# Kernel tuning notes

Measured on AMD Instinct MI355X. Metric: run time of the kernel, lower is better.

Reference implementation:

```python
import jax, jax.numpy as jnp
import numpy as np

N, E, F_IN, H, G, C = 50000, 800000, 128, 4, 32, 4
NEG_SLOPE = 0.2
EPS_GN = 1e-5


def setup_inputs() -> dict:
    key = jax.random.key(0)
    ks = iter(jax.random.split(key, 64))
    def gl(shape, fan):
        return jax.random.normal(next(ks), shape, jnp.float32) / np.float32(np.sqrt(fan))
    inp = {}
    inp['x'] = jax.random.normal(next(ks), (N, F_IN), jnp.float32)
    inp['edge_index'] = jax.random.randint(next(ks), (2, E), 0, N, dtype=jnp.int32)
    inp['batch'] = jnp.sort(jax.random.randint(next(ks), (N,), 0, G, dtype=jnp.int32))
    inp['Wl1'] = gl((F_IN, H * 64), F_IN); inp['bl1'] = jnp.zeros((H * 64,), jnp.float32)
    inp['Wr1'] = gl((F_IN, H * 64), F_IN); inp['br1'] = jnp.zeros((H * 64,), jnp.float32)
    inp['att1'] = gl((H, 64), 64); inp['bias1'] = jnp.zeros((H * 64,), jnp.float32)
    inp['gw1'] = jnp.ones((H * 64,), jnp.float32); inp['gb1'] = jnp.zeros((H * 64,), jnp.float32); inp['ga1'] = jnp.ones((H * 64,), jnp.float32)
    inp['Wl2'] = gl((256, H * 32), 256); inp['bl2'] = jnp.zeros((H * 32,), jnp.float32)
    inp['Wr2'] = gl((256, H * 32), 256); inp['br2'] = jnp.zeros((H * 32,), jnp.float32)
    inp['att2'] = gl((H, 32), 32); inp['bias2'] = jnp.zeros((H * 32,), jnp.float32)
    inp['gw2'] = jnp.ones((H * 32,), jnp.float32); inp['gb2'] = jnp.zeros((H * 32,), jnp.float32); inp['ga2'] = jnp.ones((H * 32,), jnp.float32)
    # GATv2 layer 3: 128 -> 16, 4 heads averaged (concat=False)
    inp['Wl3'] = gl((128, H * 16), 128); inp['bl3'] = jnp.zeros((H * 16,), jnp.float32)
    inp['Wr3'] = gl((128, H * 16), 128); inp['br3'] = jnp.zeros((H * 16,), jnp.float32)
    inp['att3'] = gl((H, 16), 16); inp['bias3'] = jnp.zeros((16,), jnp.float32)
    inp['gw3'] = jnp.ones((16,), jnp.float32); inp['gb3'] = jnp.zeros((16,), jnp.float32); inp['ga3'] = jnp.ones((16,), jnp.float32)
    # final linear 16 -> C
    inp['linW'] = gl((16, C), 16); inp['linB'] = jnp.zeros((C,), jnp.float32)
    return inp


def _gatv2(x, src, dst, Wl, bl, Wr, br, att, bias, D, concat):
    n = x.shape[0]
    xl = (x @ Wl + bl).reshape(n, H, D)   # source-side transform
    xr = (x @ Wr + br).reshape(n, H, D)   # target-side transform
    m = xl[src] + xr[dst]                  # [E', H, D]
    s = jnp.einsum('ehd,hd->eh', jax.nn.leaky_relu(m, NEG_SLOPE), att)
    smax = jax.ops.segment_max(s, dst, num_segments=n)
    e = jnp.exp(s - smax[dst])
    denom = jax.ops.segment_sum(e, dst, num_segments=n)
    alpha = e / (denom[dst] + 1e-16)       # softmax over incoming edges
    out = jax.ops.segment_sum(alpha[:, :, None] * xl[src], dst, num_segments=n)
    out = out.reshape(n, H * D) if concat else out.mean(axis=1)
    return out + bias


def _graphnorm(x, batch, w, b, a):
    cnt = jnp.maximum(jax.ops.segment_sum(jnp.ones((x.shape[0],), x.dtype), batch, num_segments=G), 1.0)
    mean = jax.ops.segment_sum(x, batch, num_segments=G) / cnt[:, None]
    xc = x - a * mean[batch]
    var = jax.ops.segment_sum(xc * xc, batch, num_segments=G) / cnt[:, None]
    return w * xc / jnp.sqrt(var[batch] + EPS_GN) + b


def reference(x, edge_index, batch,
              Wl1, bl1, Wr1, br1, att1, bias1, gw1, gb1, ga1,
              Wl2, bl2, Wr2, br2, att2, bias2, gw2, gb2, ga2,
              Wl3, bl3, Wr3, br3, att3, bias3, gw3, gb3, ga3,
              linW, linB):
    n = x.shape[0]
    ar = jnp.arange(n, dtype=edge_index.dtype)
    src = jnp.concatenate([edge_index[0], ar])  # add self-loops (PyG default)
    dst = jnp.concatenate([edge_index[1], ar])
    h = jax.nn.relu(_graphnorm(_gatv2(x, src, dst, Wl1, bl1, Wr1, br1, att1, bias1, 64, True), batch, gw1, gb1, ga1))
    h = jax.nn.relu(_graphnorm(_gatv2(h, src, dst, Wl2, bl2, Wr2, br2, att2, bias2, 32, True), batch, gw2, gb2, ga2))
    h = jax.nn.relu(_graphnorm(_gatv2(h, src, dst, Wl3, bl3, Wr3, br3, att3, bias3, 16, False), batch, gw3, gb3, ga3))
    cnt = jnp.maximum(jax.ops.segment_sum(jnp.ones((n,), h.dtype), batch, num_segments=G), 1.0)
    features = jax.ops.segment_sum(h, batch, num_segments=G) / cnt[:, None]  # global mean pool [G,16]
    logits = features @ linW + linB
    return (logits, features)
```

## Files before the change

kernel.cpp:

```cpp
#include <hip/hip_runtime.h>
#include <cstdint>


#define NEG_SLOPE 0.2f

typedef __attribute__((ext_vector_type(8))) short short8;
typedef __attribute__((ext_vector_type(4))) float f32x4;
typedef _Float16 h2 __attribute__((ext_vector_type(2)));
union U16 { uint4 u; short8 s; };

__device__ inline unsigned short f2bf_rne(float x) {
  unsigned u = __float_as_uint(x);
  return (unsigned short)((u + 0x7fff + ((u >> 16) & 1)) >> 16);
}
__device__ inline unsigned short f2h_bits(float x) {
  _Float16 h = (_Float16)x;
  return __builtin_bit_cast(unsigned short, h);
}
__device__ inline float h2f(unsigned short h) {
  return (float)__builtin_bit_cast(_Float16, h);
}
__device__ inline h2 u2h2(unsigned u) { return __builtin_bit_cast(h2, u); }

__device__ inline float fdot2h(h2 a, h2 b, float c) {
#if __has_builtin(__builtin_amdgcn_fdot2)
  return __builtin_amdgcn_fdot2(a, b, c, false);
#else
  return c + (float)a.x * (float)b.x + (float)a.y * (float)b.y;
#endif
}

__device__ inline int wave_incl_scan(int v, int lane) {
#pragma unroll
  for (int ofs = 1; ofs < 64; ofs <<= 1) {
    int t = __shfl_up(v, ofs, 64);
    if (lane >= ofs) v += t;
  }
  return v;
}

__global__ void deg_hist(const int* __restrict__ ei, int* __restrict__ deg, int E, int N) {
  int i = blockIdx.x * blockDim.x + threadIdx.x;
  int ET = E + N;
  if (i >= ET) return;
  int d = (i < E) ? ei[E + i] : (i - E);
  atomicAdd(&deg[d], 1);
}

__global__ void chunk_sums(const int* __restrict__ deg, int* __restrict__ bsum, int n) {
  int tid = threadIdx.x, lane = tid & 63, wid = tid >> 6;
  int i = blockIdx.x * 1024 + tid;
  int v = (i < n) ? deg[i] : 0;
#pragma unroll
  for (int m = 32; m; m >>= 1) v += __shfl_xor(v, m, 64);
  __shared__ int ws[16];
  if (lane == 0) ws[wid] = v;
  __syncthreads();
  if (tid == 0) {
    int s = 0;
    for (int k = 0; k < 16; ++k) s += ws[k];
    bsum[blockIdx.x] = s;
  }
}

__global__ void scan_small(int* __restrict__ bsum, int* __restrict__ off, int nb, int n) {
  int lane = threadIdx.x;
  int v = (lane < nb) ? bsum[lane] : 0;
  int orig = v;
  int incl = wave_incl_scan(v, lane);
  if (lane < nb) bsum[lane] = incl - orig;
  if (lane == nb - 1) off[n] = incl;
}

__global__ void scan_apply(const int* __restrict__ deg, const int* __restrict__ boff,
                           int* __restrict__ off, int n) {
  int tid = threadIdx.x, lane = tid & 63, wid = tid >> 6;
  int i = blockIdx.x * 1024 + tid;
  int v = (i < n) ? deg[i] : 0;
  int incl = wave_incl_scan(v, lane);
  __shared__ int ws[16];
  if (lane == 63) ws[wid] = incl;
  __syncthreads();
  if (wid == 0) {
    int t = (lane < 16) ? ws[lane] : 0;
    t = wave_incl_scan(t, lane);
    if (lane < 16) ws[lane] = t;
  }
  __syncthreads();
  int wpre = (wid > 0) ? ws[wid - 1] : 0;
  if (i < n) off[i] = boff[blockIdx.x] + wpre + incl - v;
}

__global__ void scatter_edges(const int* __restrict__ ei, const int* __restrict__ off,
                              int* __restrict__ cur, int* __restrict__ csr_src,
                              int E, int N) {
  int i = blockIdx.x * blockDim.x + threadIdx.x;
  int ET = E + N;
  if (i >= ET) return;
  int s, d;
  if (i < E) { s = ei[i]; d = ei[E + i]; } else { s = d = i - E; }
  int pos = off[d] + atomicAdd(&cur[d], 1);
  csr_src[pos] = s;
}

__global__ void batch_hist(const int* __restrict__ batch, int* __restrict__ cnt, int n) {
  __shared__ int h[32];
  if (threadIdx.x < 32) h[threadIdx.x] = 0;
  __syncthreads();
  int i = blockIdx.x * blockDim.x + threadIdx.x;
  if (i < n) atomicAdd(&h[batch[i]], 1);
  __syncthreads();
  if (threadIdx.x < 32 && h[threadIdx.x] > 0) atomicAdd(&cnt[threadIdx.x], h[threadIdx.x]);
}

__global__ void wprep(const float* __restrict__ W, unsigned short* __restrict__ pk,
                      int K, int M) {
  int t = blockIdx.x * blockDim.x + threadIdx.x;
  int nk = K >> 5;
  int total = (M >> 4) * nk * 512;
  if (t >= total) return;
  int j = t & 7;
  int l = (t >> 3) & 63;
  int rest = t >> 9;
  int kc = rest % nk;
  int ct = rest / nk;
  int k = (kc << 5) + ((l >> 4) << 3) + j;
  int col = (ct << 4) + (l & 15);
  float w = W[(size_t)k * M + col];
  unsigned u = __float_as_uint(w);
  unsigned short hi = (unsigned short)(u >> 16);
  float hif = __uint_as_float(u & 0xffff0000u);
  unsigned short lo = f2bf_rne(w - hif);
  unsigned short* dst = pk + ((size_t)(ct * nk + kc) * 64 + l) * 16;
  dst[j] = hi;
  dst[j + 8] = lo;
}

__global__ __launch_bounds__(256) void gemm_mfma_f32a(
    const float* __restrict__ A, const uint4* __restrict__ Wpk,
    const float* __restrict__ bias, unsigned short* __restrict__ C,
    int N, int K, int M) {
  int wv = threadIdx.x >> 6, lane = threadIdx.x & 63;
  int r0 = blockIdx.y * 64 + wv * 16;
  int c0g = blockIdx.x << 2;
  int row = r0 + (lane & 15);
  int kq = (lane >> 4) << 3;
  int nk = K >> 5;
  bool rok = row < N;
  const float* arow = A + (size_t)row * K;
  f32x4 acc[4];
#pragma unroll
  for (int i = 0; i < 4; ++i) acc[i] = (f32x4){0.f, 0.f, 0.f, 0.f};
  for (int kc = 0; kc < nk; ++kc) {
    float av[8];
    if (rok) {
      float4 t0 = *(const float4*)(arow + (kc << 5) + kq);
      float4 t1 = *(const float4*)(arow + (kc << 5) + kq + 4);
      av[0] = t0.x; av[1] = t0.y; av[2] = t0.z; av[3] = t0.w;
      av[4] = t1.x; av[5] = t1.y; av[6] = t1.z; av[7] = t1.w;
    } else {
#pragma unroll
      for (int j = 0; j < 8; ++j) av[j] = 0.f;
    }
    short8 ahi, alo;
#pragma unroll
    for (int j = 0; j < 8; ++j) {
      unsigned u = __float_as_uint(av[j]);
      ahi[j] = (short)(u >> 16);
      float hif = __uint_as_float(u & 0xffff0000u);
      alo[j] = (short)f2bf_rne(av[j] - hif);
    }
#pragma unroll
    for (int ct = 0; ct < 4; ++ct) {
      const uint4* p = Wpk + (((size_t)(c0g + ct) * nk + kc) * 64 + lane) * 2;
      U16 bh, bl;
      bh.u = p[0];
      bl.u = p[1];
      acc[ct] = __builtin_amdgcn_mfma_f32_16x16x32_bf16(alo, bh.s, acc[ct], 0, 0, 0);
      acc[ct] = __builtin_amdgcn_mfma_f32_16x16x32_bf16(ahi, bl.s, acc[ct], 0, 0, 0);
      acc[ct] = __builtin_amdgcn_mfma_f32_16x16x32_bf16(ahi, bh.s, acc[ct], 0, 0, 0);
    }
  }
  int orow0 = r0 + ((lane >> 4) << 2);
  int ocol = (c0g << 4) + (lane & 15);
#pragma unroll
  for (int ct = 0; ct < 4; ++ct) {
    int col = ocol + (ct << 4);
    float bv = bias[col];
#pragma unroll
    for (int r = 0; r < 4; ++r) {
      int gr = orow0 + r;
      if (gr < N) C[(size_t)gr * M + col] = f2h_bits(acc[ct][r] + bv);
    }
  }
}

__global__ __launch_bounds__(256) void gemm_mfma_bf16a(
    const unsigned short* __restrict__ A, const uint4* __restrict__ Wpk,
    const float* __restrict__ bias, unsigned short* __restrict__ C,
    int N, int K, int M) {
  int wv = threadIdx.x >> 6, lane = threadIdx.x & 63;
  int r0 = blockIdx.y * 64 + wv * 16;
  int c0g = blockIdx.x << 2;
  int row = r0 + (lane & 15);
  int kq = (lane >> 4) << 3;
  int nk = K >> 5;
  bool rok = row < N;
  const unsigned short* arow = A + (size_t)row * K;
  f32x4 acc[4];
#pragma unroll
  for (int i = 0; i < 4; ++i) acc[i] = (f32x4){0.f, 0.f, 0.f, 0.f};
  for (int kc = 0; kc < nk; ++kc) {
    short8 a;
    if (rok) {
      a = *(const short8*)(arow + (kc << 5) + kq);
    } else {
#pragma unroll
      for (int j = 0; j < 8; ++j) a[j] = 0;
    }
#pragma unroll
    for (int ct = 0; ct < 4; ++ct) {
      const uint4* p = Wpk + (((size_t)(c0g + ct) * nk + kc) * 64 + lane) * 2;
      U16 bh, bl;
      bh.u = p[0];
      bl.u = p[1];
      acc[ct] = __builtin_amdgcn_mfma_f32_16x16x32_bf16(a, bl.s, acc[ct], 0, 0, 0);
      acc[ct] = __builtin_amdgcn_mfma_f32_16x16x32_bf16(a, bh.s, acc[ct], 0, 0, 0);
    }
  }
  int orow0 = r0 + ((lane >> 4) << 2);
  int ocol = (c0g << 4) + (lane & 15);
#pragma unroll
  for (int ct = 0; ct < 4; ++ct) {
    int col = ocol + (ct << 4);
    float bv = bias[col];
#pragma unroll
    for (int r = 0; r < 4; ++r) {
      int gr = orow0 + r;
      if (gr < N) C[(size_t)gr * M + col] = f2h_bits(acc[ct][r] + bv);
    }
  }
}

template <int VEC> struct EO;

template <> struct EO<4> {
  using R = uint2;
  h2 xr0, xr1, at0, at1, sl;
  __device__ void init(const unsigned short* xrp, const float* ap) {
    uint2 rr = *(const uint2*)xrp;
    xr0 = u2h2(rr.x); xr1 = u2h2(rr.y);
    float4 a = *(const float4*)ap;
    at0 = (h2){(_Float16)a.x, (_Float16)a.y};
    at1 = (h2){(_Float16)a.z, (_Float16)a.w};
    sl = (h2){(_Float16)NEG_SLOPE, (_Float16)NEG_SLOPE};
  }
  static __device__ R ld(const unsigned short* base, size_t off) {
    return *(const uint2*)(base + off);
  }
  __device__ float score(R r) const {
    h2 t0 = u2h2(r.x) + xr0;
    h2 t1 = u2h2(r.y) + xr1;
    t0 = __builtin_elementwise_max(t0, t0 * sl);
    t1 = __builtin_elementwise_max(t1, t1 * sl);
    return fdot2h(t0, at0, fdot2h(t1, at1, 0.f));
  }
  static __device__ void accum(R r, float p, float* o) {
    h2 x0 = u2h2(r.x), x1 = u2h2(r.y);
    o[0] = fmaf(p, (float)x0.x, o[0]);
    o[1] = fmaf(p, (float)x0.y, o[1]);
    o[2] = fmaf(p, (float)x1.x, o[2]);
    o[3] = fmaf(p, (float)x1.y, o[3]);
  }
};

template <> struct EO<2> {
  using R = unsigned;
  h2 xr0, at0, sl;
  __device__ void init(const unsigned short* xrp, const float* ap) {
    xr0 = u2h2(*(const unsigned*)xrp);
    float2 a = *(const float2*)ap;
    at0 = (h2){(_Float16)a.x, (_Float16)a.y};
    sl = (h2){(_Float16)NEG_SLOPE, (_Float16)NEG_SLOPE};
  }
  static __device__ R ld(const unsigned short* base, size_t off) {
    return *(const unsigned*)(base + off);
  }
  __device__ float score(R r) const {
    h2 t0 = u2h2(r) + xr0;
    t0 = __builtin_elementwise_max(t0, t0 * sl);
    return fdot2h(t0, at0, 0.f);
  }
  static __device__ void accum(R r, float p, float* o) {
    h2 x0 = u2h2(r);
    o[0] = fmaf(p, (float)x0.x, o[0]);
    o[1] = fmaf(p, (float)x0.y, o[1]);
  }
};

template <> struct EO<1> {
  using R = unsigned short;
  float xrf, atf;
  __device__ void init(const unsigned short* xrp, const float* ap) {
    xrf = h2f(*xrp);
    atf = *ap;
  }
  static __device__ R ld(const unsigned short* base, size_t off) {
    return base[off];
  }
  __device__ float score(R r) const {
    float t = h2f(r) + xrf;
    float lk = fmaxf(t, NEG_SLOPE * t);
    return lk * atf;
  }
  static __device__ void accum(R r, float p, float* o) {
    o[0] = fmaf(p, h2f(r), o[0]);
  }
};

template <int VEC, bool MEANH, bool OUT16>
__global__ __launch_bounds__(256) void gat_fused(
    const unsigned short* __restrict__ xl, const unsigned short* __restrict__ xr,
    const float* __restrict__ att, const int* __restrict__ csr_src,
    const int* __restrict__ offp, const float* __restrict__ bias,
    void* __restrict__ outv, int n) {
  constexpr int HD = VEC * 64;
  int wave = (int)((blockIdx.x * (size_t)blockDim.x + threadIdx.x) >> 6);
  int lane = threadIdx.x & 63;
  if (wave >= n) return;
  const int f0 = lane * VEC;

  EO<VEC> eo;
  eo.init(xr + (size_t)wave * HD + f0, att + f0);

  float lrun = 0.f;
  float o[VEC];
#pragma unroll
  for (int v = 0; v < VEC; ++v) o[v] = 0.f;

  int beg = __builtin_amdgcn_readfirstlane(offp[wave]);
  int end = __builtin_amdgcn_readfirstlane(offp[wave + 1]);
  int j = beg;
  int endf = beg + ((end - beg) & ~3);

  for (; j < endf; j += 4) {
    int s0 = csr_src[j], s1 = csr_src[j + 1], s2 = csr_src[j + 2], s3 = csr_src[j + 3];
    typename EO<VEC>::R r0 = eo.ld(xl, (size_t)s0 * HD + f0);
    typename EO<VEC>::R r1 = eo.ld(xl, (size_t)s1 * HD + f0);
    typename EO<VEC>::R r2 = eo.ld(xl, (size_t)s2 * HD + f0);
    typename EO<VEC>::R r3 = eo.ld(xl, (size_t)s3 * HD + f0);
    float sc0 = eo.score(r0), sc1 = eo.score(r1), sc2 = eo.score(r2), sc3 = eo.score(r3);
#pragma unroll
    for (int msk = 1; msk <= 8; msk <<= 1) {
      sc0 += __shfl_xor(sc0, msk, 64);
      sc1 += __shfl_xor(sc1, msk, 64);
      sc2 += __shfl_xor(sc2, msk, 64);
      sc3 += __shfl_xor(sc3, msk, 64);
    }
    float p0 = __expf(sc0), p1 = __expf(sc1);
    float p2 = __expf(sc2), p3 = __expf(sc3);
    lrun += (p0 + p1) + (p2 + p3);
    EO<VEC>::accum(r0, p0, o);
    EO<VEC>::accum(r1, p1, o);
    EO<VEC>::accum(r2, p2, o);
    EO<VEC>::accum(r3, p3, o);
  }
  for (; j < end; ++j) {
    int s0 = csr_src[j];
    typename EO<VEC>::R r0 = eo.ld(xl, (size_t)s0 * HD + f0);
    float sc0 = eo.score(r0);
#pragma unroll
    for (int msk = 1; msk <= 8; msk <<= 1) sc0 += __shfl_xor(sc0, msk, 64);
    float p0 = __expf(sc0);
    lrun += p0;
    EO<VEC>::accum(r0, p0, o);
  }

  float invl = 1.f / (lrun + 1e-16f);
  if (!MEANH) {
    if (OUT16) {
      unsigned short* out = (unsigned short*)outv;
#pragma unroll
      for (int v = 0; v < VEC; ++v)
        out[(size_t)wave * HD + f0 + v] = f2h_bits(o[v] * invl + bias[f0 + v]);
    } else {
      float* out = (float*)outv;
#pragma unroll
      for (int v = 0; v < VEC; ++v)
        out[(size_t)wave * HD + f0 + v] = o[v] * invl + bias[f0 + v];
    }
  } else {
    float val = o[0] * invl;
    val += __shfl_xor(val, 16, 64);
    val += __shfl_xor(val, 32, 64);
    val *= 0.25f;
    if (lane < 16) ((float*)outv)[(size_t)wave * 16 + lane] = val + bias[lane];
  }
}

template <int F>
__global__ void gn_stats_h(const unsigned short* __restrict__ x, const int* __restrict__ batch,
                           float* __restrict__ gsum, float* __restrict__ gsqs, int n) {
  constexpr int ROWS = 256 / F;
  int f = threadIdx.x % F;
  int r = threadIdx.x / F;
  int n0 = blockIdx.x * 128;
  float s = 0.f, q = 0.f;
  int curg = -1;
  for (int i = r; i < 128; i += ROWS) {
    int nn = n0 + i;
    if (nn >= n) break;
    int g = batch[nn];
    float v = h2f(x[(size_t)nn * F + f]);
    if (g != curg) {
      if (curg >= 0) { atomicAdd(&gsum[curg * F + f], s); atomicAdd(&gsqs[curg * F + f], q); }
      curg = g; s = 0.f; q = 0.f;
    }
    s += v; q += v * v;
  }
  if (curg >= 0) { atomicAdd(&gsum[curg * F + f], s); atomicAdd(&gsqs[curg * F + f], q); }
}

template <int F>
__global__ void gn_stats(const float* __restrict__ x, const int* __restrict__ batch,
                         float* __restrict__ gsum, float* __restrict__ gsqs, int n) {
  constexpr int ROWS = 256 / F;
  int f = threadIdx.x % F;
  int r = threadIdx.x / F;
  int n0 = blockIdx.x * 128;
  float s = 0.f, q = 0.f;
  int curg = -1;
  for (int i = r; i < 128; i += ROWS) {
    int nn = n0 + i;
    if (nn >= n) break;
    int g = batch[nn];
    float v = x[(size_t)nn * F + f];
    if (g != curg) {
      if (curg >= 0) { atomicAdd(&gsum[curg * F + f], s); atomicAdd(&gsqs[curg * F + f], q); }
      curg = g; s = 0.f; q = 0.f;
    }
    s += v; q += v * v;
  }
  if (curg >= 0) { atomicAdd(&gsum[curg * F + f], s); atomicAdd(&gsqs[curg * F + f], q); }
}

__global__ void gn_final(const float* __restrict__ gsum, const float* __restrict__ gsqs,
                         const int* __restrict__ cnt, const float* __restrict__ ga,
                         float* __restrict__ gmean, float* __restrict__ grstd, int F) {
  int idx = blockIdx.x * blockDim.x + threadIdx.x;
  if (idx >= 32 * F) return;
  int g = idx / F, f = idx % F;
  float c = fmaxf((float)cnt[g], 1.f);
  float mu = gsum[idx] / c;
  float msq = gsqs[idx] / c;
  float a = ga[f];
  float var = msq - (2.f * a - a * a) * mu * mu;
  var = fmaxf(var, 0.f);
  gmean[idx] = mu;
  grstd[idx] = rsqrtf(var + 1e-5f);
}

template <int F>
__global__ void gn_norm_h_bf16(const unsigned short* __restrict__ x, const int* __restrict__ batch,
                               const float* __restrict__ gmean, const float* __restrict__ grstd,
                               const float* __restrict__ gw, const float* __restrict__ gb,
                               const float* __restrict__ ga, unsigned short* __restrict__ xo,
                               int n) {
  int idx = blockIdx.x * blockDim.x + threadIdx.x;
  if (idx >= n * F) return;
  int nn = idx / F;
  int f = idx % F;
  int g = batch[nn];
  float v = h2f(x[idx]);
  float y = gw[f] * (v - ga[f] * gmean[g * F + f]) * grstd[g * F + f] + gb[f];
  xo[idx] = f2bf_rne(fmaxf(y, 0.f));
}

template <int F>
__global__ void gn_norm(float* __restrict__ x, const int* __restrict__ batch,
                        const float* __restrict__ gmean, const float* __restrict__ grstd,
                        const float* __restrict__ gw, const float* __restrict__ gb,
                        const float* __restrict__ ga, int n) {
  int idx = blockIdx.x * blockDim.x + threadIdx.x;
  if (idx >= n * F) return;
  int nn = idx / F;
  int f = idx % F;
  int g = batch[nn];
  float v = x[idx];
  float y = gw[f] * (v - ga[f] * gmean[g * F + f]) * grstd[g * F + f] + gb[f];
  x[idx] = fmaxf(y, 0.f);
}

__global__ void pool_sum(const float* __restrict__ x, const int* __restrict__ batch,
                         float* __restrict__ pooled, int n) {
  int f = threadIdx.x & 15;
  int r = threadIdx.x >> 4;
  int n0 = blockIdx.x * 128;
  float s = 0.f;
  int curg = -1;
  for (int i = r; i < 128; i += 16) {
    int nn = n0 + i;
    if (nn >= n) break;
    int g = batch[nn];
    float v = x[(size_t)nn * 16 + f];
    if (g != curg) {
      if (curg >= 0) atomicAdd(&pooled[curg * 16 + f], s);
      curg = g; s = 0.f;
    }
    s += v;
  }
  if (curg >= 0) atomicAdd(&pooled[curg * 16 + f], s);
}

__global__ void finalize(const float* __restrict__ pooled, const int* __restrict__ cnt,
                         const float* __restrict__ linW, const float* __restrict__ linB,
                         float* __restrict__ out) {
  __shared__ float feat[32 * 16];
  int tid = threadIdx.x;
  {
    int g = tid >> 4;
    float c = fmaxf((float)cnt[g], 1.f);
    float v = pooled[tid] / c;
    feat[tid] = v;
    out[128 + tid] = v;
  }
  __syncthreads();
  if (tid < 128) {
    int g = tid >> 2, c = tid & 3;
    float s = linB[c];
#pragma unroll
    for (int k = 0; k < 16; ++k) s += feat[g * 16 + k] * linW[k * 4 + c];
    out[g * 4 + c] = s;
  }
}

extern "C" void kernel_launch(void* const* d_in, const int* in_sizes, int n_in,
                              void* d_out, int out_size, void* d_ws, size_t ws_size,
                              hipStream_t stream) {
  const float* x     = (const float*)d_in[0];
  const int*   ei    = (const int*)d_in[1];
  const int*   batch = (const int*)d_in[2];
  const float* Wl1 = (const float*)d_in[3];
  const float* bl1 = (const float*)d_in[4];
  const float* Wr1 = (const float*)d_in[5];
  const float* br1 = (const float*)d_in[6];
  const float* att1 = (const float*)d_in[7];
  const float* bias1 = (const float*)d_in[8];
  const float* gw1 = (const float*)d_in[9];
  const float* gb1 = (const float*)d_in[10];
  const float* ga1 = (const float*)d_in[11];
  const float* Wl2 = (const float*)d_in[12];
  const float* bl2 = (const float*)d_in[13];
  const float* Wr2 = (const float*)d_in[14];
  const float* br2 = (const float*)d_in[15];
  const float* att2 = (const float*)d_in[16];
  const float* bias2 = (const float*)d_in[17];
  const float* gw2 = (const float*)d_in[18];
  const float* gb2 = (const float*)d_in[19];
  const float* ga2 = (const float*)d_in[20];
  const float* Wl3 = (const float*)d_in[21];
  const float* bl3 = (const float*)d_in[22];
  const float* Wr3 = (const float*)d_in[23];
  const float* br3 = (const float*)d_in[24];
  const float* att3 = (const float*)d_in[25];
  const float* bias3 = (const float*)d_in[26];
  const float* gw3 = (const float*)d_in[27];
  const float* gb3 = (const float*)d_in[28];
  const float* ga3 = (const float*)d_in[29];
  const float* linW = (const float*)d_in[30];
  const float* linB = (const float*)d_in[31];
  float* out = (float*)d_out;

  const int N  = in_sizes[2];
  const int E  = in_sizes[1] / 2;
  const int ET = E + N;

  char* w = (char*)d_ws;
  float* P = (float*)w;             w += (size_t)N * 256 * 4;
  unsigned short* Ph = (unsigned short*)P;
  unsigned short* Pb = (unsigned short*)w; w += (size_t)N * 256 * 2;
  unsigned short* Qb = (unsigned short*)w; w += (size_t)N * 256 * 2;
  unsigned short* Rb = (unsigned short*)w; w += (size_t)N * 256 * 2;
  int* csr_src = (int*)w;           w += (size_t)ET * 4;
  int* deg  = (int*)w;              w += (size_t)N * 4;
  int* offp = (int*)w;              w += (size_t)(N + 1) * 4;
  int* cur  = (int*)w;              w += (size_t)N * 4;
  int* bsum = (int*)w;              w += 64 * 4;
  int* cnt  = (int*)w;              w += 32 * 4;
  float* gsum  = (float*)w;         w += 32 * 256 * 4;
  float* gsqs  = (float*)w;         w += 32 * 256 * 4;
  float* gmean = (float*)w;         w += 32 * 256 * 4;
  float* grstd = (float*)w;         w += 32 * 256 * 4;
  float* pooled = (float*)w;        w += 512 * 4;
  uintptr_t wal = ((uintptr_t)w + 15) & ~(uintptr_t)15;
  uint4* wpk1l = (uint4*)wal;
  uint4* wpk1r = wpk1l + 8192;
  uint4* wpk2l = wpk1r + 8192;
  uint4* wpk2r = wpk2l + 8192;
  uint4* wpk3l = wpk2r + 8192;
  uint4* wpk3r = wpk3l + 2048;

  (void)hipMemsetAsync(deg, 0, sizeof(int) * N, stream);
  (void)hipMemsetAsync(cur, 0, sizeof(int) * N, stream);
  (void)hipMemsetAsync(cnt, 0, sizeof(int) * 32, stream);
  (void)hipMemsetAsync(pooled, 0, sizeof(float) * 512, stream);

  wprep<<<128, 256, 0, stream>>>(Wl1, (unsigned short*)wpk1l, 128, 256);
  wprep<<<128, 256, 0, stream>>>(Wr1, (unsigned short*)wpk1r, 128, 256);
  wprep<<<128, 256, 0, stream>>>(Wl2, (unsigned short*)wpk2l, 256, 128);
  wprep<<<128, 256, 0, stream>>>(Wr2, (unsigned short*)wpk2r, 256, 128);
  wprep<<<32, 256, 0, stream>>>(Wl3, (unsigned short*)wpk3l, 128, 64);
  wprep<<<32, 256, 0, stream>>>(Wr3, (unsigned short*)wpk3r, 128, 64);

  int nb = (N + 1023) / 1024;
  deg_hist<<<(ET + 255) / 256, 256, 0, stream>>>(ei, deg, E, N);
  chunk_sums<<<nb, 1024, 0, stream>>>(deg, bsum, N);
  scan_small<<<1, 64, 0, stream>>>(bsum, offp, nb, N);
  scan_apply<<<nb, 1024, 0, stream>>>(deg, bsum, offp, N);
  scatter_edges<<<(ET + 255) / 256, 256, 0, stream>>>(ei, offp, cur, csr_src, E, N);
  batch_hist<<<(N + 255) / 256, 256, 0, stream>>>(batch, cnt, N);

  int gry = (N + 63) / 64;
  {
    gemm_mfma_f32a<<<dim3(4, gry), 256, 0, stream>>>(x, wpk1l, bl1, Qb, N, 128, 256);
    gemm_mfma_f32a<<<dim3(4, gry), 256, 0, stream>>>(x, wpk1r, br1, Rb, N, 128, 256);
    gat_fused<4, false, true><<<(N + 3) / 4, 256, 0, stream>>>(Qb, Rb, att1, csr_src, offp, bias1, Ph, N);
    (void)hipMemsetAsync(gsum, 0, sizeof(float) * 2 * 32 * 256, stream);
    gn_stats_h<256><<<(N + 127) / 128, 256, 0, stream>>>(Ph, batch, gsum, gsqs, N);
    gn_final<<<(32 * 256 + 255) / 256, 256, 0, stream>>>(gsum, gsqs, cnt, ga1, gmean, grstd, 256);
    gn_norm_h_bf16<256><<<(int)(((size_t)N * 256 + 255) / 256), 256, 0, stream>>>(Ph, batch, gmean, grstd, gw1, gb1, ga1, Pb, N);
  }
  {
    gemm_mfma_bf16a<<<dim3(2, gry), 256, 0, stream>>>(Pb, wpk2l, bl2, Qb, N, 256, 128);
    gemm_mfma_bf16a<<<dim3(2, gry), 256, 0, stream>>>(Pb, wpk2r, br2, Rb, N, 256, 128);
    gat_fused<2, false, true><<<(N + 3) / 4, 256, 0, stream>>>(Qb, Rb, att2, csr_src, offp, bias2, Ph, N);
    (void)hipMemsetAsync(gsum, 0, sizeof(float) * 2 * 32 * 256, stream);
    gn_stats_h<128><<<(N + 127) / 128, 256, 0, stream>>>(Ph, batch, gsum, gsqs, N);
    gn_final<<<(32 * 128 + 255) / 256, 256, 0, stream>>>(gsum, gsqs, cnt, ga2, gmean, grstd, 128);
    gn_norm_h_bf16<128><<<(int)(((size_t)N * 128 + 255) / 256), 256, 0, stream>>>(Ph, batch, gmean, grstd, gw2, gb2, ga2, Pb, N);
  }
  {
    gemm_mfma_bf16a<<<dim3(1, gry), 256, 0, stream>>>(Pb, wpk3l, bl3, Qb, N, 128, 64);
    gemm_mfma_bf16a<<<dim3(1, gry), 256, 0, stream>>>(Pb, wpk3r, br3, Rb, N, 128, 64);
    gat_fused<1, true, false><<<(N + 3) / 4, 256, 0, stream>>>(Qb, Rb, att3, csr_src, offp, bias3, P, N);
    (void)hipMemsetAsync(gsum, 0, sizeof(float) * 2 * 32 * 256, stream);
    gn_stats<16><<<(N + 127) / 128, 256, 0, stream>>>(P, batch, gsum, gsqs, N);
    gn_final<<<(32 * 16 + 255) / 256, 256, 0, stream>>>(gsum, gsqs, cnt, ga3, gmean, grstd, 16);
    gn_norm<16><<<(int)(((size_t)N * 16 + 255) / 256), 256, 0, stream>>>(P, batch, gmean, grstd, gw3, gb3, ga3, N);
  }
  pool_sum<<<(N + 127) / 128, 256, 0, stream>>>(P, batch, pooled, N);
  finalize<<<1, 512, 0, stream>>>(pooled, cnt, linW, linB, out);
}
```

Measured before the change: 736.4 us.

## Fuse preprocessing kernels, dual-output GEMMs, and inline GraphNorm finalization

Merges the degree and batch histograms, the six weight-prep launches, and the scan kernels, and replaces the separate memsets with one contiguous memset. Each layer's left and right GEMMs now run as one kernel sharing the A loads. GraphNorm stat zeroing moves into gat_fused and gn_final is folded into the normalize kernels. The edge loop is unrolled to 8-edge chunks. The goal is fewer launches and less redundant A traffic, at the cost of more registers in the dual GEMM and recomputing mean and rstd per element.

Result: faster. 663.1 us (-10.0%).

```diff
diff --git a/kernel.cpp b/kernel.cpp
--- a/kernel.cpp
+++ b/kernel.cpp
@@ -39,12 +39,20 @@
   return v;
 }
 
-__global__ void deg_hist(const int* __restrict__ ei, int* __restrict__ deg, int E, int N) {
+__global__ void deg_batch_hist(const int* __restrict__ ei, const int* __restrict__ batch,
+                               int* __restrict__ deg, int* __restrict__ cnt, int E, int N) {
+  __shared__ int h[32];
+  if (threadIdx.x < 32) h[threadIdx.x] = 0;
+  __syncthreads();
   int i = blockIdx.x * blockDim.x + threadIdx.x;
   int ET = E + N;
-  if (i >= ET) return;
-  int d = (i < E) ? ei[E + i] : (i - E);
-  atomicAdd(&deg[d], 1);
+  if (i < ET) {
+    int d = (i < E) ? ei[E + i] : (i - E);
+    atomicAdd(&deg[d], 1);
+  }
+  if (i < N) atomicAdd(&h[batch[i]], 1);
+  __syncthreads();
+  if (threadIdx.x < 32 && h[threadIdx.x] > 0) atomicAdd(&cnt[threadIdx.x], h[threadIdx.x]);
 }
 
 __global__ void chunk_sums(const int* __restrict__ deg, int* __restrict__ bsum, int n) {
@@ -63,22 +71,22 @@
   }
 }
 
-__global__ void scan_small(int* __restrict__ bsum, int* __restrict__ off, int nb, int n) {
-  int lane = threadIdx.x;
-  int v = (lane < nb) ? bsum[lane] : 0;
-  int orig = v;
-  int incl = wave_incl_scan(v, lane);
-  if (lane < nb) bsum[lane] = incl - orig;
-  if (lane == nb - 1) off[n] = incl;
-}
-
-__global__ void scan_apply(const int* __restrict__ deg, const int* __restrict__ boff,
-                           int* __restrict__ off, int n) {
+__global__ void scan_apply(const int* __restrict__ deg, const int* __restrict__ bsum,
+                           int* __restrict__ off, int nb, int n) {
+  __shared__ int ws[16];
+  __shared__ int sb[64];
   int tid = threadIdx.x, lane = tid & 63, wid = tid >> 6;
+  if (wid == 0) {
+    int v = (lane < nb) ? bsum[lane] : 0;
+    int incl = wave_incl_scan(v, lane);
+    sb[lane] = incl;
+  }
+  __syncthreads();
+  int boff = (blockIdx.x > 0) ? sb[blockIdx.x - 1] : 0;
+  if (blockIdx.x == 0 && tid == 0) off[n] = sb[nb - 1];
   int i = blockIdx.x * 1024 + tid;
   int v = (i < n) ? deg[i] : 0;
   int incl = wave_incl_scan(v, lane);
-  __shared__ int ws[16];
   if (lane == 63) ws[wid] = incl;
   __syncthreads();
   if (wid == 0) {
@@ -88,7 +96,7 @@
   }
   __syncthreads();
   int wpre = (wid > 0) ? ws[wid - 1] : 0;
-  if (i < n) off[i] = boff[blockIdx.x] + wpre + incl - v;
+  if (i < n) off[i] = boff + wpre + incl - v;
 }
 
 __global__ void scatter_edges(const int* __restrict__ ei, const int* __restrict__ off,
@@ -103,19 +111,8 @@
   csr_src[pos] = s;
 }
 
-__global__ void batch_hist(const int* __restrict__ batch, int* __restrict__ cnt, int n) {
-  __shared__ int h[32];
-  if (threadIdx.x < 32) h[threadIdx.x] = 0;
-  __syncthreads();
-  int i = blockIdx.x * blockDim.x + threadIdx.x;
-  if (i < n) atomicAdd(&h[batch[i]], 1);
-  __syncthreads();
-  if (threadIdx.x < 32 && h[threadIdx.x] > 0) atomicAdd(&cnt[threadIdx.x], h[threadIdx.x]);
-}
-
-__global__ void wprep(const float* __restrict__ W, unsigned short* __restrict__ pk,
-                      int K, int M) {
-  int t = blockIdx.x * blockDim.x + threadIdx.x;
+__device__ inline void wprep_body(const float* __restrict__ W, unsigned short* __restrict__ pk,
+                                  int K, int M, int t) {
   int nk = K >> 5;
   int total = (M >> 4) * nk * 512;
   if (t >= total) return;
@@ -136,9 +133,26 @@
   dst[j + 8] = lo;
 }
 
-__global__ __launch_bounds__(256) void gemm_mfma_f32a(
-    const float* __restrict__ A, const uint4* __restrict__ Wpk,
-    const float* __restrict__ bias, unsigned short* __restrict__ C,
+__global__ void wprep_all(const float* W0, const float* W1, const float* W2,
+                          const float* W3, const float* W4, const float* W5,
+                          unsigned short* p0, unsigned short* p1, unsigned short* p2,
+                          unsigned short* p3, unsigned short* p4, unsigned short* p5) {
+  int t = blockIdx.x * 256 + threadIdx.x;
+  switch (blockIdx.y) {
+    case 0: wprep_body(W0, p0, 128, 256, t); break;
+    case 1: wprep_body(W1, p1, 128, 256, t); break;
+    case 2: wprep_body(W2, p2, 256, 128, t); break;
+    case 3: wprep_body(W3, p3, 256, 128, t); break;
+    case 4: wprep_body(W4, p4, 128, 64, t); break;
+    default: wprep_body(W5, p5, 128, 64, t); break;
+  }
+}
+
+__global__ __launch_bounds__(256) void gemm_f32a_dual(
+    const float* __restrict__ A,
+    const uint4* __restrict__ WpkL, const uint4* __restrict__ WpkR,
+    const float* __restrict__ biasL, const float* __restrict__ biasR,
+    unsigned short* __restrict__ CL, unsigned short* __restrict__ CR,
     int N, int K, int M) {
   int wv = threadIdx.x >> 6, lane = threadIdx.x & 63;
   int r0 = blockIdx.y * 64 + wv * 16;
@@ -148,9 +162,9 @@
   int nk = K >> 5;
   bool rok = row < N;
   const float* arow = A + (size_t)row * K;
-  f32x4 acc[4];
-#pragma unroll
-  for (int i = 0; i < 4; ++i) acc[i] = (f32x4){0.f, 0.f, 0.f, 0.f};
+  f32x4 accL[4], accR[4];
+#pragma unroll
+  for (int i = 0; i < 4; ++i) { accL[i] = (f32x4){0,0,0,0}; accR[i] = (f32x4){0,0,0,0}; }
   for (int kc = 0; kc < nk; ++kc) {
     float av[8];
     if (rok) {
@@ -172,13 +186,16 @@
     }
 #pragma unroll
     for (int ct = 0; ct < 4; ++ct) {
-      const uint4* p = Wpk + (((size_t)(c0g + ct) * nk + kc) * 64 + lane) * 2;
+      size_t fo = (((size_t)(c0g + ct) * nk + kc) * 64 + lane) * 2;
       U16 bh, bl;
-      bh.u = p[0];
-      bl.u = p[1];
-      acc[ct] = __builtin_amdgcn_mfma_f32_16x16x32_bf16(alo, bh.s, acc[ct], 0, 0, 0);
-      acc[ct] = __builtin_amdgcn_mfma_f32_16x16x32_bf16(ahi, bl.s, acc[ct], 0, 0, 0);
-      acc[ct] = __builtin_amdgcn_mfma_f32_16x16x32_bf16(ahi, bh.s, acc[ct], 0, 0, 0);
+      bh.u = WpkL[fo]; bl.u = WpkL[fo + 1];
+      accL[ct] = __builtin_amdgcn_mfma_f32_16x16x32_bf16(alo, bh.s, accL[ct], 0, 0, 0);
+      accL[ct] = __builtin_amdgcn_mfma_f32_16x16x32_bf16(ahi, bl.s, accL[ct], 0, 0, 0);
+      accL[ct] = __builtin_amdgcn_mfma_f32_16x16x32_bf16(ahi, bh.s, accL[ct], 0, 0, 0);
+      bh.u = WpkR[fo]; bl.u = WpkR[fo + 1];
+      accR[ct] = __builtin_amdgcn_mfma_f32_16x16x32_bf16(alo, bh.s, accR[ct], 0, 0, 0);
+      accR[ct] = __builtin_amdgcn_mfma_f32_16x16x32_bf16(ahi, bl.s, accR[ct], 0, 0, 0);
+      accR[ct] = __builtin_amdgcn_mfma_f32_16x16x32_bf16(ahi, bh.s, accR[ct], 0, 0, 0);
     }
   }
   int orow0 = r0 + ((lane >> 4) << 2);
@@ -186,18 +203,23 @@
 #pragma unroll
   for (int ct = 0; ct < 4; ++ct) {
     int col = ocol + (ct << 4);
-    float bv = bias[col];
+    float bvL = biasL[col], bvR = biasR[col];
 #pragma unroll
     for (int r = 0; r < 4; ++r) {
       int gr = orow0 + r;
-      if (gr < N) C[(size_t)gr * M + col] = f2h_bits(acc[ct][r] + bv);
-    }
-  }
-}
-
-__global__ __launch_bounds__(256) void gemm_mfma_bf16a(
-    const unsigned short* __restrict__ A, const uint4* __restrict__ Wpk,
-    const float* __restrict__ bias, unsigned short* __restrict__ C,
+      if (gr < N) {
+        CL[(size_t)gr * M + col] = f2h_bits(accL[ct][r] + bvL);
+        CR[(size_t)gr * M + col] = f2h_bits(accR[ct][r] + bvR);
+      }
+    }
+  }
+}
+
+__global__ __launch_bounds__(256) void gemm_bf16a_dual(
+    const unsigned short* __restrict__ A,
+    const uint4* __restrict__ WpkL, const uint4* __restrict__ WpkR,
+    const float* __restrict__ biasL, const float* __restrict__ biasR,
+    unsigned short* __restrict__ CL, unsigned short* __restrict__ CR,
     int N, int K, int M) {
   int wv = threadIdx.x >> 6, lane = threadIdx.x & 63;
   int r0 = blockIdx.y * 64 + wv * 16;
@@ -207,9 +229,9 @@
   int nk = K >> 5;
   bool rok = row < N;
   const unsigned short* arow = A + (size_t)row * K;
-  f32x4 acc[4];
-#pragma unroll
-  for (int i = 0; i < 4; ++i) acc[i] = (f32x4){0.f, 0.f, 0.f, 0.f};
+  f32x4 accL[4], accR[4];
+#pragma unroll
+  for (int i = 0; i < 4; ++i) { accL[i] = (f32x4){0,0,0,0}; accR[i] = (f32x4){0,0,0,0}; }
   for (int kc = 0; kc < nk; ++kc) {
     short8 a;
     if (rok) {
@@ -220,12 +242,14 @@
     }
 #pragma unroll
     for (int ct = 0; ct < 4; ++ct) {
-      const uint4* p = Wpk + (((size_t)(c0g + ct) * nk + kc) * 64 + lane) * 2;
+      size_t fo = (((size_t)(c0g + ct) * nk + kc) * 64 + lane) * 2;
       U16 bh, bl;
-      bh.u = p[0];
-      bl.u = p[1];
-      acc[ct] = __builtin_amdgcn_mfma_f32_16x16x32_bf16(a, bl.s, acc[ct], 0, 0, 0);
-      acc[ct] = __builtin_amdgcn_mfma_f32_16x16x32_bf16(a, bh.s, acc[ct], 0, 0, 0);
+      bh.u = WpkL[fo]; bl.u = WpkL[fo + 1];
+      accL[ct] = __builtin_amdgcn_mfma_f32_16x16x32_bf16(a, bl.s, accL[ct], 0, 0, 0);
+      accL[ct] = __builtin_amdgcn_mfma_f32_16x16x32_bf16(a, bh.s, accL[ct], 0, 0, 0);
+      bh.u = WpkR[fo]; bl.u = WpkR[fo + 1];
+      accR[ct] = __builtin_amdgcn_mfma_f32_16x16x32_bf16(a, bl.s, accR[ct], 0, 0, 0);
+      accR[ct] = __builtin_amdgcn_mfma_f32_16x16x32_bf16(a, bh.s, accR[ct], 0, 0, 0);
     }
   }
   int orow0 = r0 + ((lane >> 4) << 2);
@@ -233,11 +257,14 @@
 #pragma unroll
   for (int ct = 0; ct < 4; ++ct) {
     int col = ocol + (ct << 4);
-    float bv = bias[col];
+    float bvL = biasL[col], bvR = biasR[col];
 #pragma unroll
     for (int r = 0; r < 4; ++r) {
       int gr = orow0 + r;
-      if (gr < N) C[(size_t)gr * M + col] = f2h_bits(acc[ct][r] + bv);
+      if (gr < N) {
+        CL[(size_t)gr * M + col] = f2h_bits(accL[ct][r] + bvL);
+        CR[(size_t)gr * M + col] = f2h_bits(accR[ct][r] + bvR);
+      }
     }
   }
 }
@@ -318,13 +345,43 @@
   }
 };
 
+template <int VEC, int C>
+__device__ inline void gat_chunk(const unsigned short* __restrict__ xl,
+                                 const int* __restrict__ csr_src, int j, int f0,
+                                 const EO<VEC>& eo, float& lrun, float* o) {
+  constexpr int HD = VEC * 64;
+  typename EO<VEC>::R r[C];
+#pragma unroll
+  for (int c = 0; c < C; ++c)
+    r[c] = EO<VEC>::ld(xl, (size_t)csr_src[j + c] * HD + f0);
+  float sc[C];
+#pragma unroll
+  for (int c = 0; c < C; ++c) sc[c] = eo.score(r[c]);
+#pragma unroll
+  for (int msk = 1; msk <= 8; msk <<= 1)
+#pragma unroll
+    for (int c = 0; c < C; ++c) sc[c] += __shfl_xor(sc[c], msk, 64);
+  float p[C];
+#pragma unroll
+  for (int c = 0; c < C; ++c) p[c] = __expf(sc[c]);
+#pragma unroll
+  for (int c = 0; c < C; ++c) lrun += p[c];
+#pragma unroll
+  for (int c = 0; c < C; ++c) EO<VEC>::accum(r[c], p[c], o);
+}
+
 template <int VEC, bool MEANH, bool OUT16>
 __global__ __launch_bounds__(256) void gat_fused(
     const unsigned short* __restrict__ xl, const unsigned short* __restrict__ xr,
     const float* __restrict__ att, const int* __restrict__ csr_src,
     const int* __restrict__ offp, const float* __restrict__ bias,
-    void* __restrict__ outv, int n) {
+    void* __restrict__ outv, float* __restrict__ gsz, float* __restrict__ gqz,
+    int n) {
   constexpr int HD = VEC * 64;
+  {
+    int zt = blockIdx.x * 256 + threadIdx.x;
+    if (zt < 32 * 256) { gsz[zt] = 0.f; gqz[zt] = 0.f; }
+  }
   int wave = (int)((blockIdx.x * (size_t)blockDim.x + threadIdx.x) >> 6);
   int lane = threadIdx.x & 63;
   if (wave >= n) return;
@@ -341,40 +398,9 @@
   int beg = __builtin_amdgcn_readfirstlane(offp[wave]);
   int end = __builtin_amdgcn_readfirstlane(offp[wave + 1]);
   int j = beg;
-  int endf = beg + ((end - beg) & ~3);
-
-  for (; j < endf; j += 4) {
-    int s0 = csr_src[j], s1 = csr_src[j + 1], s2 = csr_src[j + 2], s3 = csr_src[j + 3];
-    typename EO<VEC>::R r0 = eo.ld(xl, (size_t)s0 * HD + f0);
-    typename EO<VEC>::R r1 = eo.ld(xl, (size_t)s1 * HD + f0);
-    typename EO<VEC>::R r2 = eo.ld(xl, (size_t)s2 * HD + f0);
-    typename EO<VEC>::R r3 = eo.ld(xl, (size_t)s3 * HD + f0);
-    float sc0 = eo.score(r0), sc1 = eo.score(r1), sc2 = eo.score(r2), sc3 = eo.score(r3);
-#pragma unroll
-    for (int msk = 1; msk <= 8; msk <<= 1) {
-      sc0 += __shfl_xor(sc0, msk, 64);
-      sc1 += __shfl_xor(sc1, msk, 64);
-      sc2 += __shfl_xor(sc2, msk, 64);
-      sc3 += __shfl_xor(sc3, msk, 64);
-    }
-    float p0 = __expf(sc0), p1 = __expf(sc1);
-    float p2 = __expf(sc2), p3 = __expf(sc3);
-    lrun += (p0 + p1) + (p2 + p3);
-    EO<VEC>::accum(r0, p0, o);
-    EO<VEC>::accum(r1, p1, o);
-    EO<VEC>::accum(r2, p2, o);
-    EO<VEC>::accum(r3, p3, o);
-  }
-  for (; j < end; ++j) {
-    int s0 = csr_src[j];
-    typename EO<VEC>::R r0 = eo.ld(xl, (size_t)s0 * HD + f0);
-    float sc0 = eo.score(r0);
-#pragma unroll
-    for (int msk = 1; msk <= 8; msk <<= 1) sc0 += __shfl_xor(sc0, msk, 64);
-    float p0 = __expf(sc0);
-    lrun += p0;
-    EO<VEC>::accum(r0, p0, o);
-  }
+  for (; j + 8 <= end; j += 8) gat_chunk<VEC, 8>(xl, csr_src, j, f0, eo, lrun, o);
+  if (j + 4 <= end) { gat_chunk<VEC, 4>(xl, csr_src, j, f0, eo, lrun, o); j += 4; }
+  for (; j < end; ++j) gat_chunk<VEC, 1>(xl, csr_src, j, f0, eo, lrun, o);
 
   float invl = 1.f / (lrun + 1e-16f);
   if (!MEANH) {
@@ -444,25 +470,10 @@
   if (curg >= 0) { atomicAdd(&gsum[curg * F + f], s); atomicAdd(&gsqs[curg * F + f], q); }
 }
 
-__global__ void gn_final(const float* __restrict__ gsum, const float* __restrict__ gsqs,
-                         const int* __restrict__ cnt, const float* __restrict__ ga,
-                         float* __restrict__ gmean, float* __restrict__ grstd, int F) {
-  int idx = blockIdx.x * blockDim.x + threadIdx.x;
-  if (idx >= 32 * F) return;
-  int g = idx / F, f = idx % F;
-  float c = fmaxf((float)cnt[g], 1.f);
-  float mu = gsum[idx] / c;
-  float msq = gsqs[idx] / c;
-  float a = ga[f];
-  float var = msq - (2.f * a - a * a) * mu * mu;
-  var = fmaxf(var, 0.f);
-  gmean[idx] = mu;
-  grstd[idx] = rsqrtf(var + 1e-5f);
-}
-
 template <int F>
 __global__ void gn_norm_h_bf16(const unsigned short* __restrict__ x, const int* __restrict__ batch,
-                               const float* __restrict__ gmean, const float* __restrict__ grstd,
+                               const float* __restrict__ gsum, const float* __restrict__ gsqs,
+                               const int* __restrict__ cnt,
                                const float* __restrict__ gw, const float* __restrict__ gb,
                                const float* __restrict__ ga, unsigned short* __restrict__ xo,
                                int n) {
@@ -471,14 +482,20 @@
   int nn = idx / F;
   int f = idx % F;
   int g = batch[nn];
+  float c = fmaxf((float)cnt[g], 1.f);
+  float a = ga[f];
+  float mu = gsum[g * F + f] / c;
+  float var = fmaxf(gsqs[g * F + f] / c - (2.f * a - a * a) * mu * mu, 0.f);
+  float rstd = rsqrtf(var + 1e-5f);
   float v = h2f(x[idx]);
-  float y = gw[f] * (v - ga[f] * gmean[g * F + f]) * grstd[g * F + f] + gb[f];
+  float y = gw[f] * (v - a * mu) * rstd + gb[f];
   xo[idx] = f2bf_rne(fmaxf(y, 0.f));
 }
 
 template <int F>
 __global__ void gn_norm(float* __restrict__ x, const int* __restrict__ batch,
-                        const float* __restrict__ gmean, const float* __restrict__ grstd,
+                        const float* __restrict__ gsum, const float* __restrict__ gsqs,
+                        const int* __restrict__ cnt,
                         const float* __restrict__ gw, const float* __restrict__ gb,
                         const float* __restrict__ ga, int n) {
   int idx = blockIdx.x * blockDim.x + threadIdx.x;
@@ -486,8 +503,13 @@
   int nn = idx / F;
   int f = idx % F;
   int g = batch[nn];
+  float c = fmaxf((float)cnt[g], 1.f);
+  float a = ga[f];
+  float mu = gsum[g * F + f] / c;
+  float var = fmaxf(gsqs[g * F + f] / c - (2.f * a - a * a) * mu * mu, 0.f);
+  float rstd = rsqrtf(var + 1e-5f);
   float v = x[idx];
-  float y = gw[f] * (v - ga[f] * gmean[g * F + f]) * grstd[g * F + f] + gb[f];
+  float y = gw[f] * (v - a * mu) * rstd + gb[f];
   x[idx] = fmaxf(y, 0.f);
 }
 
@@ -582,16 +604,16 @@
   unsigned short* Qb = (unsigned short*)w; w += (size_t)N * 256 * 2;
   unsigned short* Rb = (unsigned short*)w; w += (size_t)N * 256 * 2;
   int* csr_src = (int*)w;           w += (size_t)ET * 4;
+  int* offp = (int*)w;              w += (size_t)(N + 1) * 4;
+  int* bsum = (int*)w;              w += 64 * 4;
+  char* z0 = w;
   int* deg  = (int*)w;              w += (size_t)N * 4;
-  int* offp = (int*)w;              w += (size_t)(N + 1) * 4;
   int* cur  = (int*)w;              w += (size_t)N * 4;
-  int* bsum = (int*)w;              w += 64 * 4;
   int* cnt  = (int*)w;              w += 32 * 4;
+  float* pooled = (float*)w;        w += 512 * 4;
   float* gsum  = (float*)w;         w += 32 * 256 * 4;
   float* gsqs  = (float*)w;         w += 32 * 256 * 4;
-  float* gmean = (float*)w;         w += 32 * 256 * 4;
-  float* grstd = (float*)w;         w += 32 * 256 * 4;
-  float* pooled = (float*)w;        w += 512 * 4;
+  size_t zbytes = (size_t)(w - z0);
   uintptr_t wal = ((uintptr_t)w + 15) & ~(uintptr_t)15;
   uint4* wpk1l = (uint4*)wal;
   uint4* wpk1r = wpk1l + 8192;
@@ -600,53 +622,38 @@
   uint4* wpk3l = wpk2r + 8192;
   uint4* wpk3r = wpk3l + 2048;
 
-  (void)hipMemsetAsync(deg, 0, sizeof(int) * N, stream);
-  (void)hipMemsetAsync(cur, 0, sizeof(int) * N, stream);
-  (void)hipMemsetAsync(cnt, 0, sizeof(int) * 32, stream);
-  (void)hipMemsetAsync(pooled, 0, sizeof(float) * 512, stream);
-
-  wprep<<<128, 256, 0, stream>>>(Wl1, (unsigned short*)wpk1l, 128, 256);
-  wprep<<<128, 256, 0, stream>>>(Wr1, (unsigned short*)wpk1r, 128, 256);
-  wprep<<<128, 256, 0, stream>>>(Wl2, (unsigned short*)wpk2l, 256, 128);
-  wprep<<<128, 256, 0, stream>>>(Wr2, (unsigned short*)wpk2r, 256, 128);
-  wprep<<<32, 256, 0, stream>>>(Wl3, (unsigned short*)wpk3l, 128, 64);
-  wprep<<<32, 256, 0, stream>>>(Wr3, (unsigned short*)wpk3r, 128, 64);
+  (void)hipMemsetAsync(z0, 0, zbytes, stream);
+
+  wprep_all<<<dim3(128, 6), 256, 0, stream>>>(
+      Wl1, Wr1, Wl2, Wr2, Wl3, Wr3,
+      (unsigned short*)wpk1l, (unsigned short*)wpk1r,
+      (unsigned short*)wpk2l, (unsigned short*)wpk2r,
+      (unsigned short*)wpk3l, (unsigned short*)wpk3r);
 
   int nb = (N + 1023) / 1024;
-  deg_hist<<<(ET + 255) / 256, 256, 0, stream>>>(ei, deg, E, N);
+  deg_batch_hist<<<(ET + 255) / 256, 256, 0, stream>>>(ei, batch, deg, cnt, E, N);
   chunk_sums<<<nb, 1024, 0, stream>>>(deg, bsum, N);
-  scan_small<<<1, 64, 0, stream>>>(bsum, offp, nb, N);
-  scan_apply<<<nb, 1024, 0, stream>>>(deg, bsum, offp, N);
+  scan_apply<<<nb, 1024, 0, stream>>>(deg, bsum, offp, nb, N);
   scatter_edges<<<(ET + 255) / 256, 256, 0, stream>>>(ei, offp, cur, csr_src, E, N);
-  batch_hist<<<(N + 255) / 256, 256, 0, stream>>>(batch, cnt, N);
 
   int gry = (N + 63) / 64;
   {
-    gemm_mfma_f32a<<<dim3(4, gry), 256, 0, stream>>>(x, wpk1l, bl1, Qb, N, 128, 256);
-    gemm_mfma_f32a<<<dim3(4, gry), 256, 0, stream>>>(x, wpk1r, br1, Rb, N, 128, 256);
-    gat_fused<4, false, true><<<(N + 3) / 4, 256, 0, stream>>>(Qb, Rb, att1, csr_src, offp, bias1, Ph, N);
-    (void)hipMemsetAsync(gsum, 0, sizeof(float) * 2 * 32 * 256, stream);
+    gemm_f32a_dual<<<dim3(4, gry), 256, 0, stream>>>(x, wpk1l, wpk1r, bl1, br1, Qb, Rb, N, 128, 256);
+    gat_fused<4, false, true><<<(N + 3) / 4, 256, 0, stream>>>(Qb, Rb, att1, csr_src, offp, bias1, Ph, gsum, gsqs, N);
     gn_stats_h<256><<<(N + 127) / 128, 256, 0, stream>>>(Ph, batch, gsum, gsqs, N);
-    gn_final<<<(32 * 256 + 255) / 256, 256, 0, stream>>>(gsum, gsqs, cnt, ga1, gmean, grstd, 256);
-    gn_norm_h_bf16<256><<<(int)(((size_t)N * 256 + 255) / 256), 256, 0, stream>>>(Ph, batch, gmean, grstd, gw1, gb1, ga1, Pb, N);
+    gn_norm_h_bf16<256><<<(int)(((size_t)N * 256 + 255) / 256), 256, 0, stream>>>(Ph, batch, gsum, gsqs, cnt, gw1, gb1, ga1, Pb, N);
   }
   {
-    gemm_mfma_bf16a<<<dim3(2, gry), 256, 0, stream>>>(Pb, wpk2l, bl2, Qb, N, 256, 128);
-    gemm_mfma_bf16a<<<dim3(2, gry), 256, 0, stream>>>(Pb, wpk2r, br2, Rb, N, 256, 128);
-    gat_fused<2, false, true><<<(N + 3) / 4, 256, 0, stream>>>(Qb, Rb, att2, csr_src, offp, bias2, Ph, N);
-    (void)hipMemsetAsync(gsum, 0, sizeof(float) * 2 * 32 * 256, stream);
+    gemm_bf16a_dual<<<dim3(2, gry), 256, 0, stream>>>(Pb, wpk2l, wpk2r, bl2, br2, Qb, Rb, N, 256, 128);
+    gat_fused<2, false, true><<<(N + 3) / 4, 256, 0, stream>>>(Qb, Rb, att2, csr_src, offp, bias2, Ph, gsum, gsqs, N);
     gn_stats_h<128><<<(N + 127) / 128, 256, 0, stream>>>(Ph, batch, gsum, gsqs, N);
-    gn_final<<<(32 * 128 + 255) / 256, 256, 0, stream>>>(gsum, gsqs, cnt, ga2, gmean, grstd, 128);
-    gn_norm_h_bf16<128><<<(int)(((size_t)N * 128 + 255) / 256), 256, 0, stream>>>(Ph, batch, gmean, grstd, gw2, gb2, ga2, Pb, N);
+    gn_norm_h_bf16<128><<<(int)(((size_t)N * 128 + 255) / 256), 256, 0, stream>>>(Ph, batch, gsum, gsqs, cnt, gw2, gb2, ga2, Pb, N);
   }
   {
-    gemm_mfma_bf16a<<<dim3(1, gry), 256, 0, stream>>>(Pb, wpk3l, bl3, Qb, N, 128, 64);
-    gemm_mfma_bf16a<<<dim3(1, gry), 256, 0, stream>>>(Pb, wpk3r, br3, Rb, N, 128, 64);
-    gat_fused<1, true, false><<<(N + 3) / 4, 256, 0, stream>>>(Qb, Rb, att3, csr_src, offp, bias3, P, N);
-    (void)hipMemsetAsync(gsum, 0, sizeof(float) * 2 * 32 * 256, stream);
+    gemm_bf16a_dual<<<dim3(1, gry), 256, 0, stream>>>(Pb, wpk3l, wpk3r, bl3, br3, Qb, Rb, N, 128, 64);
+    gat_fused<1, true, false><<<(N + 3) / 4, 256, 0, stream>>>(Qb, Rb, att3, csr_src, offp, bias3, P, gsum, gsqs, N);
     gn_stats<16><<<(N + 127) / 128, 256, 0, stream>>>(P, batch, gsum, gsqs, N);
-    gn_final<<<(32 * 16 + 255) / 256, 256, 0, stream>>>(gsum, gsqs, cnt, ga3, gmean, grstd, 16);
-    gn_norm<16><<<(int)(((size_t)N * 16 + 255) / 256), 256, 0, stream>>>(P, batch, gmean, grstd, gw3, gb3, ga3, N);
+    gn_norm<16><<<(int)(((size_t)N * 16 + 255) / 256), 256, 0, stream>>>(P, batch, gsum, gsqs, cnt, gw3, gb3, ga3, N);
   }
   pool_sum<<<(N + 127) / 128, 256, 0, stream>>>(P, batch, pooled, N);
   finalize<<<1, 512, 0, stream>>>(pooled, cnt, linW, linB, out);
```
